# Kernel optimization log

Measured on AMD Instinct MI355X. Metric: run time of the kernel, lower is better.

The kernel has to match this reference:

```python
import jax, jax.numpy as jnp
import numpy as np

D_KQ = 1024

def setup_inputs() -> dict:
    key = jax.random.key(0)
    k1, k2, k3, k4, k5 = jax.random.split(key, 5)
    x = jax.random.normal(k1, (4, 2048, 1024), dtype=jnp.float32)
    attention_mask = jax.random.randint(k2, (2048, 2048), 0, 2) == 1
    q_weights = jax.random.normal(k3, (1024, 1024), dtype=jnp.float32)
    k_weights = jax.random.normal(k4, (1024, 1024), dtype=jnp.float32)
    v_weights = jax.random.normal(k5, (1024, 1024), dtype=jnp.float32)
    return {"x": x, "attention_mask": attention_mask,
            "q_weights": q_weights, "k_weights": k_weights, "v_weights": v_weights}

def reference(x, attention_mask, q_weights, k_weights, v_weights):
    # projections: [B,S,d_in] @ [d_in,d] -> [B,S,d]
    query = x @ q_weights
    key = x @ k_weights
    value = x @ v_weights
    # scores: [B,S,S]
    attn_scores = jnp.einsum('bqd,bkd->bqk', query, key)
    masked = jnp.where(attention_mask, -jnp.inf, attn_scores)
    attn_weights = jax.nn.softmax(masked / jnp.sqrt(jnp.float32(D_KQ)), axis=-1)
    return attn_weights @ value
```

## Files before the change

### kernel.cpp

```cpp
#include <hip/hip_runtime.h>
#include <math.h>

static constexpr int BATCH = 4;
static constexpr int SEQ   = 2048;
static constexpr int DIM   = 1024;

typedef __attribute__((ext_vector_type(8))) short     bf16x8;
typedef __attribute__((ext_vector_type(4))) float     f32x4;

__device__ __forceinline__ unsigned short f2b(float v) {
    unsigned int u = __float_as_uint(v);
    u = u + 0x7fffu + ((u >> 16) & 1u);
    return (unsigned short)(u >> 16);
}
__device__ __forceinline__ float b2f(unsigned short h) {
    return __uint_as_float(((unsigned int)h) << 16);
}

__global__ __launch_bounds__(256) void convert_x_kernel(
    const float* __restrict__ X, unsigned short* __restrict__ hi,
    unsigned short* __restrict__ lo)
{
    const int i = blockIdx.x * 256 + threadIdx.x;
    const float4 v = ((const float4*)X)[i];
    ushort4 h, l;
    h.x = f2b(v.x); l.x = f2b(v.x - b2f(h.x));
    h.y = f2b(v.y); l.y = f2b(v.y - b2f(h.y));
    h.z = f2b(v.z); l.z = f2b(v.z - b2f(h.z));
    h.w = f2b(v.w); l.w = f2b(v.w - b2f(h.w));
    ((ushort4*)hi)[i] = h;
    ((ushort4*)lo)[i] = l;
}

__global__ __launch_bounds__(256) void convert_wqk_kernel(
    const float* __restrict__ Wq, const float* __restrict__ Wk,
    unsigned short* __restrict__ hi, unsigned short* __restrict__ lo)
{
    const int z = blockIdx.y;
    const float* __restrict__ W = z ? Wk : Wq;
    const int i = blockIdx.x * 256 + threadIdx.x;
    const int o = z * (DIM * DIM / 4) + i;
    const float4 v = ((const float4*)W)[i];
    ushort4 h, l;
    h.x = f2b(v.x); l.x = f2b(v.x - b2f(h.x));
    h.y = f2b(v.y); l.y = f2b(v.y - b2f(h.y));
    h.z = f2b(v.z); l.z = f2b(v.z - b2f(h.z));
    h.w = f2b(v.w); l.w = f2b(v.w - b2f(h.w));
    ((ushort4*)hi)[o] = h;
    ((ushort4*)lo)[o] = l;
}

__global__ __launch_bounds__(256) void convert_wv_kernel(
    const float* __restrict__ W, unsigned short* __restrict__ WT)
{
    __shared__ float t[32][33];
    const int n0 = blockIdx.x * 32, k0 = blockIdx.y * 32;
    const int tx = threadIdx.x & 31, ty = threadIdx.x >> 5;
#pragma unroll
    for (int i = 0; i < 4; ++i)
        t[ty + i * 8][tx] = W[(size_t)(k0 + ty + i * 8) * DIM + (n0 + tx)];
    __syncthreads();
#pragma unroll
    for (int i = 0; i < 4; ++i)
        WT[(size_t)(n0 + ty + i * 8) * DIM + (k0 + tx)] = f2b(t[tx][ty + i * 8]);
}

__global__ __launch_bounds__(256) void mask_pack_kernel(
    const int* __restrict__ mask, unsigned long long* __restrict__ Mb)
{
    const int row  = blockIdx.x;
    const int lane = threadIdx.x & 63, w = threadIdx.x >> 6;
#pragma unroll
    for (int c = w; c < SEQ / 64; c += 4) {
        const int v = mask[(size_t)row * SEQ + c * 64 + lane];
        const unsigned long long bits = __ballot(v != 0);
        if (lane == 0) Mb[(size_t)row * (SEQ / 64) + c] = bits;
    }
}

__device__ __forceinline__ void stage_async(
    const unsigned short* __restrict__ g, int gstride, int row0, int k0,
    unsigned short* lds, int tid)
{
    const int w = tid >> 6, lane = tid & 63;
    const int c = (lane & 3) ^ ((lane >> 4) & 3);
#pragma unroll
    for (int h = 0; h < 2; ++h) {
        const int row = 32 * w + 16 * h + (lane >> 2);
        const unsigned short* src = g + (size_t)(row0 + row) * gstride + k0 + 8 * c;
        unsigned short* dst = lds + (32 * w + 16 * h) * 32;
        __builtin_amdgcn_global_load_lds(
            (const __attribute__((address_space(1))) void*)src,
            (__attribute__((address_space(3))) void*)dst, 16, 0, 0);
    }
}

__device__ __forceinline__ void stage128(
    const unsigned short* __restrict__ g, int gstride, int row0, int k0,
    unsigned short* lds, int tid)
{
    const int w = tid >> 6, lane = tid & 63;
    const int c = (lane & 3) ^ ((lane >> 4) & 3);
    const int row = 16 * w + (lane >> 2);
    const unsigned short* src = g + (size_t)(row0 + row) * gstride + k0 + 8 * c;
    unsigned short* dst = lds + (16 * w) * 32;
    __builtin_amdgcn_global_load_lds(
        (const __attribute__((address_space(1))) void*)src,
        (__attribute__((address_space(3))) void*)dst, 16, 0, 0);
}

__device__ __forceinline__ bf16x8 fragr(const unsigned short* lds, int row, int qsw)
{
    return *(const bf16x8*)(lds + row * 32 + qsw * 8);
}

__global__ __launch_bounds__(256) void m_gemm_kernel(
    const unsigned short* __restrict__ Whi, const unsigned short* __restrict__ Wlo,
    float* __restrict__ Mtp)
{
    __shared__ unsigned short Ah[128 * 32], Al[128 * 32];
    __shared__ unsigned short Bh[128 * 32], Bl[128 * 32];

    const int tid = threadIdx.x;
    const int w = tid >> 6, lane = tid & 63;
    const int wm = (w >> 1) * 64, wn = (w & 1) * 64;
    const int m0 = blockIdx.y * 128, n0 = blockIdx.x * 128;
    const int z = blockIdx.z;

    const unsigned short* __restrict__ Ahg = Whi + (size_t)DIM * DIM;
    const unsigned short* __restrict__ Alg = Wlo + (size_t)DIM * DIM;
    const unsigned short* __restrict__ Bhg = Whi;
    const unsigned short* __restrict__ Blg = Wlo;
    float* __restrict__ Cp = Mtp + (size_t)z * DIM * DIM;

    f32x4 acc[4][4];
#pragma unroll
    for (int i = 0; i < 4; ++i)
#pragma unroll
        for (int j = 0; j < 4; ++j) acc[i][j] = (f32x4){0.f, 0.f, 0.f, 0.f};

    const int fr = lane & 15, quad = lane >> 4;
    const int qsw = quad ^ ((fr >> 2) & 3);

    for (int k0 = z * 256; k0 < z * 256 + 256; k0 += 32) {
        stage_async(Ahg, DIM, m0, k0, Ah, tid);
        stage_async(Alg, DIM, m0, k0, Al, tid);
        stage_async(Bhg, DIM, n0, k0, Bh, tid);
        stage_async(Blg, DIM, n0, k0, Bl, tid);
        __syncthreads();

        bf16x8 ah[4], al[4];
#pragma unroll
        for (int mt = 0; mt < 4; ++mt) {
            ah[mt] = fragr(Ah, wm + mt * 16 + fr, qsw);
            al[mt] = fragr(Al, wm + mt * 16 + fr, qsw);
        }
#pragma unroll
        for (int nt = 0; nt < 4; ++nt) {
            const bf16x8 bh = fragr(Bh, wn + nt * 16 + fr, qsw);
            const bf16x8 bl = fragr(Bl, wn + nt * 16 + fr, qsw);
#pragma unroll
            for (int mt = 0; mt < 4; ++mt) {
                acc[mt][nt] = __builtin_amdgcn_mfma_f32_16x16x32_bf16(ah[mt], bh, acc[mt][nt], 0, 0, 0);
                acc[mt][nt] = __builtin_amdgcn_mfma_f32_16x16x32_bf16(ah[mt], bl, acc[mt][nt], 0, 0, 0);
                acc[mt][nt] = __builtin_amdgcn_mfma_f32_16x16x32_bf16(al[mt], bh, acc[mt][nt], 0, 0, 0);
            }
        }
        __syncthreads();
    }

    const int col = lane & 15, rq = lane >> 4;
#pragma unroll
    for (int mt = 0; mt < 4; ++mt)
#pragma unroll
        for (int nt = 0; nt < 4; ++nt)
#pragma unroll
            for (int e = 0; e < 4; ++e) {
                const int m = m0 + wm + mt * 16 + rq * 4 + e;
                const int n = n0 + wn + nt * 16 + col;
                Cp[(size_t)m * DIM + n] = acc[mt][nt][e];
            }
}

__global__ __launch_bounds__(256) void m_reduce_kernel(
    const float* __restrict__ Mtp, unsigned short* __restrict__ Mthi,
    unsigned short* __restrict__ Mtlo)
{
    const int i = blockIdx.x * 256 + threadIdx.x;
    const size_t q = (size_t)DIM * DIM / 4;
    const float4 a = ((const float4*)Mtp)[i];
    const float4 b = ((const float4*)Mtp)[i + q];
    const float4 c = ((const float4*)Mtp)[i + 2 * q];
    const float4 d = ((const float4*)Mtp)[i + 3 * q];
    const float4 v = make_float4(a.x + b.x + c.x + d.x, a.y + b.y + c.y + d.y,
                                 a.z + b.z + c.z + d.z, a.w + b.w + c.w + d.w);
    ushort4 h, l;
    h.x = f2b(v.x); l.x = f2b(v.x - b2f(h.x));
    h.y = f2b(v.y); l.y = f2b(v.y - b2f(h.y));
    h.z = f2b(v.z); l.z = f2b(v.z - b2f(h.z));
    h.w = f2b(v.w); l.w = f2b(v.w - b2f(h.w));
    ((ushort4*)Mthi)[i] = h;
    ((ushort4*)Mtlo)[i] = l;
}

__global__ __launch_bounds__(512, 2) void yv_gemm_kernel(
    const unsigned short* __restrict__ Xhi, const unsigned short* __restrict__ Xlo,
    const unsigned short* __restrict__ Mthi, const unsigned short* __restrict__ Mtlo,
    const unsigned short* __restrict__ WvT,
    unsigned short* __restrict__ Yhi, unsigned short* __restrict__ Ylo,
    unsigned short* __restrict__ Vt)
{
    extern __shared__ unsigned short smem[];

    const int tid = threadIdx.x;
    const int w = tid >> 6, lane = tid & 63;
    const int wm = (w >> 1) * 64, wn = (w & 1) * 64;

    const int flat = blockIdx.x + (blockIdx.y << 3);
    const int xcd = flat & 7, s = flat >> 3;
    const int m0 = (xcd + ((s >> 3) << 3)) * 256;
    const int n0 = (s & 7) * 128;

    f32x4 accY[4][4], accV[4][4];
#pragma unroll
    for (int i = 0; i < 4; ++i)
#pragma unroll
        for (int j = 0; j < 4; ++j) {
            accY[i][j] = (f32x4){0.f, 0.f, 0.f, 0.f};
            accV[i][j] = (f32x4){0.f, 0.f, 0.f, 0.f};
        }

    const int fr = lane & 15, quad = lane >> 4;
    const int qsw = quad ^ ((fr >> 2) & 3);

    stage_async(Xhi, DIM, m0, 0, smem + 0,     tid);
    stage128(Mthi, DIM, n0, 0, smem + 16384, tid);
    stage128(Mtlo, DIM, n0, 0, smem + 20480, tid);
    stage_async(Xlo, DIM, m0, 0, smem + 8192,  tid);
    stage128(WvT,  DIM, n0, 0, smem + 24576, tid);

    bf16x8 ah[4], al[4], bh[4], bl[4], bv[4];

    for (int it = 0; it < DIM / 32 - 1; ++it) {
        const int cur = (it & 1) * 28672;
        const int nxt = 28672 - cur;
        const int k1 = it * 32 + 32;

        stage_async(Xhi, DIM, m0, k1, smem + nxt, tid);
        asm volatile("s_waitcnt vmcnt(6)" ::: "memory");
        __builtin_amdgcn_s_barrier();
#pragma unroll
        for (int mt = 0; mt < 4; ++mt)
            ah[mt] = fragr(smem + cur, wm + mt * 16 + fr, qsw);
#pragma unroll
        for (int nt = 0; nt < 4; ++nt)
            bh[nt] = fragr(smem + cur + 16384, wn + nt * 16 + fr, qsw);
        __builtin_amdgcn_s_setprio(1);
#pragma unroll
        for (int nt = 0; nt < 4; ++nt)
#pragma unroll
            for (int mt = 0; mt < 4; ++mt)
                accY[mt][nt] = __builtin_amdgcn_mfma_f32_16x16x32_bf16(ah[mt], bh[nt], accY[mt][nt], 0, 0, 0);
        __builtin_amdgcn_s_setprio(0);

        stage128(Mthi, DIM, n0, k1, smem + nxt + 16384, tid);
        stage128(Mtlo, DIM, n0, k1, smem + nxt + 20480, tid);
        asm volatile("s_waitcnt vmcnt(7)" ::: "memory");
        __builtin_amdgcn_s_barrier();
#pragma unroll
        for (int nt = 0; nt < 4; ++nt)
            bl[nt] = fragr(smem + cur + 20480, wn + nt * 16 + fr, qsw);
        __builtin_amdgcn_s_setprio(1);
#pragma unroll
        for (int nt = 0; nt < 4; ++nt)
#pragma unroll
            for (int mt = 0; mt < 4; ++mt)
                accY[mt][nt] = __builtin_amdgcn_mfma_f32_16x16x32_bf16(ah[mt], bl[nt], accY[mt][nt], 0, 0, 0);
        __builtin_amdgcn_s_setprio(0);

        stage_async(Xlo, DIM, m0, k1, smem + nxt + 8192, tid);
        asm volatile("s_waitcnt vmcnt(6)" ::: "memory");
        __builtin_amdgcn_s_barrier();
#pragma unroll
        for (int nt = 0; nt < 4; ++nt)
            bv[nt] = fragr(smem + cur + 24576, wn + nt * 16 + fr, qsw);
        __builtin_amdgcn_s_setprio(1);
#pragma unroll
        for (int nt = 0; nt < 4; ++nt)
#pragma unroll
            for (int mt = 0; mt < 4; ++mt)
                accV[mt][nt] = __builtin_amdgcn_mfma_f32_16x16x32_bf16(ah[mt], bv[nt], accV[mt][nt], 0, 0, 0);
        __builtin_amdgcn_s_setprio(0);

        stage128(WvT, DIM, n0, k1, smem + nxt + 24576, tid);
        asm volatile("s_waitcnt vmcnt(8)" ::: "memory");
        __builtin_amdgcn_s_barrier();
#pragma unroll
        for (int mt = 0; mt < 4; ++mt)
            al[mt] = fragr(smem + cur + 8192, wm + mt * 16 + fr, qsw);
        __builtin_amdgcn_s_setprio(1);
#pragma unroll
        for (int nt = 0; nt < 4; ++nt)
#pragma unroll
            for (int mt = 0; mt < 4; ++mt)
                accY[mt][nt] = __builtin_amdgcn_mfma_f32_16x16x32_bf16(al[mt], bh[nt], accY[mt][nt], 0, 0, 0);
        __builtin_amdgcn_s_setprio(0);
    }

    {
        const int cur = 28672;

        asm volatile("s_waitcnt vmcnt(4)" ::: "memory");
        __builtin_amdgcn_s_barrier();
#pragma unroll
        for (int mt = 0; mt < 4; ++mt)
            ah[mt] = fragr(smem + cur, wm + mt * 16 + fr, qsw);
#pragma unroll
        for (int nt = 0; nt < 4; ++nt)
            bh[nt] = fragr(smem + cur + 16384, wn + nt * 16 + fr, qsw);
        __builtin_amdgcn_s_setprio(1);
#pragma unroll
        for (int nt = 0; nt < 4; ++nt)
#pragma unroll
            for (int mt = 0; mt < 4; ++mt)
                accY[mt][nt] = __builtin_amdgcn_mfma_f32_16x16x32_bf16(ah[mt], bh[nt], accY[mt][nt], 0, 0, 0);
        __builtin_amdgcn_s_setprio(0);

        asm volatile("s_waitcnt vmcnt(3)" ::: "memory");
        __builtin_amdgcn_s_barrier();
#pragma unroll
        for (int nt = 0; nt < 4; ++nt)
            bl[nt] = fragr(smem + cur + 20480, wn + nt * 16 + fr, qsw);
        __builtin_amdgcn_s_setprio(1);
#pragma unroll
        for (int nt = 0; nt < 4; ++nt)
#pragma unroll
            for (int mt = 0; mt < 4; ++mt)
                accY[mt][nt] = __builtin_amdgcn_mfma_f32_16x16x32_bf16(ah[mt], bl[nt], accY[mt][nt], 0, 0, 0);
        __builtin_amdgcn_s_setprio(0);

        asm volatile("s_waitcnt vmcnt(0)" ::: "memory");
        __builtin_amdgcn_s_barrier();
#pragma unroll
        for (int nt = 0; nt < 4; ++nt)
            bv[nt] = fragr(smem + cur + 24576, wn + nt * 16 + fr, qsw);
        __builtin_amdgcn_s_setprio(1);
#pragma unroll
        for (int nt = 0; nt < 4; ++nt)
#pragma unroll
            for (int mt = 0; mt < 4; ++mt)
                accV[mt][nt] = __builtin_amdgcn_mfma_f32_16x16x32_bf16(ah[mt], bv[nt], accV[mt][nt], 0, 0, 0);
        __builtin_amdgcn_s_setprio(0);

#pragma unroll
        for (int mt = 0; mt < 4; ++mt)
            al[mt] = fragr(smem + cur + 8192, wm + mt * 16 + fr, qsw);
        __builtin_amdgcn_s_setprio(1);
#pragma unroll
        for (int nt = 0; nt < 4; ++nt)
#pragma unroll
            for (int mt = 0; mt < 4; ++mt)
                accY[mt][nt] = __builtin_amdgcn_mfma_f32_16x16x32_bf16(al[mt], bh[nt], accY[mt][nt], 0, 0, 0);
        __builtin_amdgcn_s_setprio(0);
    }

    const int col = lane & 15, rq = lane >> 4;
#pragma unroll
    for (int mt = 0; mt < 4; ++mt)
#pragma unroll
        for (int nt = 0; nt < 4; ++nt)
#pragma unroll
            for (int e = 0; e < 4; ++e) {
                const int m = m0 + wm + mt * 16 + rq * 4 + e;
                const int n = n0 + wn + nt * 16 + col;
                const float v = accY[mt][nt][e];
                const unsigned short h = f2b(v);
                Yhi[(size_t)m * DIM + n] = h;
                Ylo[(size_t)m * DIM + n] = f2b(v - b2f(h));
            }
#pragma unroll
    for (int mt = 0; mt < 4; ++mt)
#pragma unroll
        for (int nt = 0; nt < 4; ++nt) {
            const int m = m0 + wm + mt * 16 + rq * 4;
            const int bb = m >> 11, sr = m & (SEQ - 1);
            const int n = n0 + wn + nt * 16 + col;
            ushort4 pk;
            pk.x = f2b(accV[mt][nt][0]);
            pk.y = f2b(accV[mt][nt][1]);
            pk.z = f2b(accV[mt][nt][2]);
            pk.w = f2b(accV[mt][nt][3]);
            *(ushort4*)(Vt + (size_t)bb * DIM * SEQ + (size_t)n * SEQ + sr) = pk;
        }
}

__global__ __launch_bounds__(512, 2) void s_gemm256_kernel(
    const unsigned short* __restrict__ Yhi, const unsigned short* __restrict__ Ylo,
    const unsigned short* __restrict__ Xhi, const unsigned short* __restrict__ Xlo,
    const unsigned long long* __restrict__ Mb, float* __restrict__ Sc)
{
    extern __shared__ unsigned short smem[];

    const int tid = threadIdx.x;
    const int w = tid >> 6, lane = tid & 63;
    const int wm = (w >> 2) * 128, wn = (w & 3) * 64;

    const int flat = blockIdx.x + (blockIdx.y << 3) + (blockIdx.z << 6);
    const int lid  = ((flat & 7) << 5) | (flat >> 3);
    const int m0 = ((lid >> 3) & 7) * 256, n0 = (lid & 7) * 256;
    const int b  = lid >> 6;

    const unsigned short* __restrict__ Ahg = Yhi + (size_t)b * SEQ * DIM;
    const unsigned short* __restrict__ Alg = Ylo + (size_t)b * SEQ * DIM;
    const unsigned short* __restrict__ Bhg = Xhi + (size_t)b * SEQ * DIM;
    const unsigned short* __restrict__ Blg = Xlo + (size_t)b * SEQ * DIM;
    float* __restrict__ Sb = Sc + (size_t)b * SEQ * SEQ;

    f32x4 acc[8][4];
#pragma unroll
    for (int i = 0; i < 8; ++i)
#pragma unroll
        for (int j = 0; j < 4; ++j) acc[i][j] = (f32x4){0.f, 0.f, 0.f, 0.f};

    const int fr = lane & 15, quad = lane >> 4;
    const int qsw = quad ^ ((fr >> 2) & 3);

    stage_async(Ahg, DIM, m0, 0, smem + 0,     tid);
    stage_async(Bhg, DIM, n0, 0, smem + 16384, tid);
    stage_async(Blg, DIM, n0, 0, smem + 24576, tid);
    stage_async(Alg, DIM, m0, 0, smem + 8192,  tid);

    for (int it = 0; it < DIM / 32 - 1; ++it) {
        const int cur = (it & 1) * 32768;
        const int nxt = cur ^ 32768;
        const unsigned short* Ah = smem + cur;
        const unsigned short* Al = smem + cur + 8192;
        const unsigned short* Bh = smem + cur + 16384;
        const unsigned short* Bl = smem + cur + 24576;
        const int k1 = it * 32 + 32;

        bf16x8 ah[8], al[8], bh[4], bl[4];

        stage_async(Ahg, DIM, m0, k1, smem + nxt, tid);
        asm volatile("s_waitcnt vmcnt(6)" ::: "memory");
        __builtin_amdgcn_s_barrier();
#pragma unroll
        for (int mt = 0; mt < 4; ++mt)
            ah[mt] = fragr(Ah, wm + mt * 16 + fr, qsw);
#pragma unroll
        for (int nt = 0; nt < 4; ++nt)
            bh[nt] = fragr(Bh, wn + nt * 16 + fr, qsw);
        __builtin_amdgcn_s_setprio(1);
#pragma unroll
        for (int nt = 0; nt < 4; ++nt)
#pragma unroll
            for (int mt = 0; mt < 4; ++mt)
                acc[mt][nt] = __builtin_amdgcn_mfma_f32_16x16x32_bf16(ah[mt], bh[nt], acc[mt][nt], 0, 0, 0);
        __builtin_amdgcn_s_setprio(0);

        stage_async(Bhg, DIM, n0, k1, smem + nxt + 16384, tid);
#pragma unroll
        for (int mt = 4; mt < 8; ++mt)
            ah[mt] = fragr(Ah, wm + mt * 16 + fr, qsw);
        __builtin_amdgcn_s_setprio(1);
#pragma unroll
        for (int nt = 0; nt < 4; ++nt)
#pragma unroll
            for (int mt = 4; mt < 8; ++mt)
                acc[mt][nt] = __builtin_amdgcn_mfma_f32_16x16x32_bf16(ah[mt], bh[nt], acc[mt][nt], 0, 0, 0);
        __builtin_amdgcn_s_setprio(0);

        stage_async(Blg, DIM, n0, k1, smem + nxt + 24576, tid);
        asm volatile("s_waitcnt vmcnt(8)" ::: "memory");
        __builtin_amdgcn_s_barrier();
#pragma unroll
        for (int nt = 0; nt < 4; ++nt)
            bl[nt] = fragr(Bl, wn + nt * 16 + fr, qsw);
        __builtin_amdgcn_s_setprio(1);
#pragma unroll
        for (int nt = 0; nt < 4; ++nt)
#pragma unroll
            for (int mt = 0; mt < 4; ++mt)
                acc[mt][nt] = __builtin_amdgcn_mfma_f32_16x16x32_bf16(ah[mt], bl[nt], acc[mt][nt], 0, 0, 0);
        __builtin_amdgcn_s_setprio(0);

        __builtin_amdgcn_s_setprio(1);
#pragma unroll
        for (int nt = 0; nt < 4; ++nt)
#pragma unroll
            for (int mt = 4; mt < 8; ++mt)
                acc[mt][nt] = __builtin_amdgcn_mfma_f32_16x16x32_bf16(ah[mt], bl[nt], acc[mt][nt], 0, 0, 0);
        __builtin_amdgcn_s_setprio(0);

        stage_async(Alg, DIM, m0, k1, smem + nxt + 8192, tid);
        asm volatile("s_waitcnt vmcnt(8)" ::: "memory");
        __builtin_amdgcn_s_barrier();
#pragma unroll
        for (int mt = 0; mt < 4; ++mt)
            al[mt] = fragr(Al, wm + mt * 16 + fr, qsw);
        __builtin_amdgcn_s_setprio(1);
#pragma unroll
        for (int nt = 0; nt < 4; ++nt)
#pragma unroll
            for (int mt = 0; mt < 4; ++mt)
                acc[mt][nt] = __builtin_amdgcn_mfma_f32_16x16x32_bf16(al[mt], bh[nt], acc[mt][nt], 0, 0, 0);
        __builtin_amdgcn_s_setprio(0);

#pragma unroll
        for (int mt = 4; mt < 8; ++mt)
            al[mt] = fragr(Al, wm + mt * 16 + fr, qsw);
        __builtin_amdgcn_s_setprio(1);
#pragma unroll
        for (int nt = 0; nt < 4; ++nt)
#pragma unroll
            for (int mt = 4; mt < 8; ++mt)
                acc[mt][nt] = __builtin_amdgcn_mfma_f32_16x16x32_bf16(al[mt], bh[nt], acc[mt][nt], 0, 0, 0);
        __builtin_amdgcn_s_setprio(0);
    }

    {
        const unsigned short* Ah = smem + 32768;
        const unsigned short* Al = smem + 32768 + 8192;
        const unsigned short* Bh = smem + 32768 + 16384;
        const unsigned short* Bl = smem + 32768 + 24576;

        bf16x8 ah[8], al[8], bh[4], bl[4];

        asm volatile("s_waitcnt vmcnt(4)" ::: "memory");
        __builtin_amdgcn_s_barrier();
#pragma unroll
        for (int mt = 0; mt < 8; ++mt)
            ah[mt] = fragr(Ah, wm + mt * 16 + fr, qsw);
#pragma unroll
        for (int nt = 0; nt < 4; ++nt)
            bh[nt] = fragr(Bh, wn + nt * 16 + fr, qsw);
        __builtin_amdgcn_s_setprio(1);
#pragma unroll
        for (int nt = 0; nt < 4; ++nt)
#pragma unroll
            for (int mt = 0; mt < 8; ++mt)
                acc[mt][nt] = __builtin_amdgcn_mfma_f32_16x16x32_bf16(ah[mt], bh[nt], acc[mt][nt], 0, 0, 0);
        __builtin_amdgcn_s_setprio(0);

        asm volatile("s_waitcnt vmcnt(2)" ::: "memory");
        __builtin_amdgcn_s_barrier();
#pragma unroll
        for (int nt = 0; nt < 4; ++nt)
            bl[nt] = fragr(Bl, wn + nt * 16 + fr, qsw);
        __builtin_amdgcn_s_setprio(1);
#pragma unroll
        for (int nt = 0; nt < 4; ++nt)
#pragma unroll
            for (int mt = 0; mt < 8; ++mt)
                acc[mt][nt] = __builtin_amdgcn_mfma_f32_16x16x32_bf16(ah[mt], bl[nt], acc[mt][nt], 0, 0, 0);
        __builtin_amdgcn_s_setprio(0);

        asm volatile("s_waitcnt vmcnt(0)" ::: "memory");
        __builtin_amdgcn_s_barrier();
#pragma unroll
        for (int mt = 0; mt < 8; ++mt)
            al[mt] = fragr(Al, wm + mt * 16 + fr, qsw);
        __builtin_amdgcn_s_setprio(1);
#pragma unroll
        for (int nt = 0; nt < 4; ++nt)
#pragma unroll
            for (int mt = 0; mt < 8; ++mt)
                acc[mt][nt] = __builtin_amdgcn_mfma_f32_16x16x32_bf16(al[mt], bh[nt], acc[mt][nt], 0, 0, 0);
        __builtin_amdgcn_s_setprio(0);
    }

    const int col = lane & 15, rq = lane >> 4;
    const int wword = (n0 + wn) >> 6;
#pragma unroll
    for (int mt = 0; mt < 8; ++mt)
#pragma unroll
        for (int e = 0; e < 4; ++e) {
            const int m = m0 + wm + mt * 16 + rq * 4 + e;
            const unsigned long long word = Mb[(size_t)m * (SEQ / 64) + wword];
#pragma unroll
            for (int nt = 0; nt < 4; ++nt) {
                const int n = n0 + wn + nt * 16 + col;
                const float v = acc[mt][nt][e] * 0.03125f;
                const bool msk = (word >> (nt * 16 + col)) & 1ull;
                Sb[(size_t)m * SEQ + n] = msk ? -INFINITY : v;
            }
        }
}

__global__ __launch_bounds__(256) void softmax_kernel(float* __restrict__ Sc)
{
    const int r = blockIdx.x;
    float* __restrict__ row = Sc + (size_t)r * SEQ;

    const int tid  = threadIdx.x;
    const int lane = tid & 63;
    const int wid  = tid >> 6;

    float x[8];
    float mx = -INFINITY;
#pragma unroll
    for (int j = 0; j < 8; ++j) {
        x[j] = row[tid + j * 256];
        mx = fmaxf(mx, x[j]);
    }
    __shared__ float redm[4];
#pragma unroll
    for (int off = 32; off > 0; off >>= 1)
        mx = fmaxf(mx, __shfl_down(mx, off, 64));
    if (lane == 0) redm[wid] = mx;
    __syncthreads();
    mx = fmaxf(fmaxf(redm[0], redm[1]), fmaxf(redm[2], redm[3]));

    float sum = 0.f;
#pragma unroll
    for (int j = 0; j < 8; ++j) {
        const float e = __expf(x[j] - mx);
        x[j] = e;
        sum += e;
    }
    __shared__ float reds[4];
#pragma unroll
    for (int off = 32; off > 0; off >>= 1)
        sum += __shfl_down(sum, off, 64);
    if (lane == 0) reds[wid] = sum;
    __syncthreads();
    sum = (reds[0] + reds[1]) + (reds[2] + reds[3]);

    const float inv = 1.0f / sum;
    unsigned short* __restrict__ prow = (unsigned short*)row;
#pragma unroll
    for (int j = 0; j < 8; ++j)
        prow[tid + j * 256] = f2b(x[j] * inv);
}

__global__ __launch_bounds__(256) void pv_mfma_kernel(
    const unsigned short* __restrict__ P, const unsigned short* __restrict__ Vt,
    float* __restrict__ O)
{
    __shared__ unsigned short As[2][128 * 32], Bs[2][128 * 32];

    const int tid = threadIdx.x;
    const int w = tid >> 6, lane = tid & 63;
    const int wm = (w >> 1) * 64, wn = (w & 1) * 64;

    const int flat = blockIdx.x + (blockIdx.y << 3) + (blockIdx.z << 7);
    const int lid  = ((flat & 7) << 6) | (flat >> 3);
    const int m0 = ((lid >> 3) & 15) * 128, n0 = (lid & 7) * 128;
    const int b  = lid >> 7;

    const unsigned short* __restrict__ Ag = P + (size_t)b * SEQ * (2 * SEQ);
    const unsigned short* __restrict__ Bg = Vt + (size_t)b * DIM * SEQ;
    float* __restrict__ Ob = O + (size_t)b * SEQ * DIM;

    f32x4 acc[4][4];
#pragma unroll
    for (int i = 0; i < 4; ++i)
#pragma unroll
        for (int j = 0; j < 4; ++j) acc[i][j] = (f32x4){0.f, 0.f, 0.f, 0.f};

    const int fr = lane & 15, quad = lane >> 4;
    const int qsw = quad ^ ((fr >> 2) & 3);

    stage_async(Ag, 2 * SEQ, m0, 0, As[0], tid);
    stage_async(Bg, SEQ,     n0, 0, Bs[0], tid);

    for (int it = 0; it < SEQ / 32 - 1; ++it) {
        const int cur = it & 1, nxt = cur ^ 1;
        const int k1 = it * 32 + 32;

        stage_async(Ag, 2 * SEQ, m0, k1, As[nxt], tid);
        stage_async(Bg, SEQ,     n0, k1, Bs[nxt], tid);
        asm volatile("s_waitcnt vmcnt(4)" ::: "memory");
        __builtin_amdgcn_s_barrier();

        bf16x8 af[4];
#pragma unroll
        for (int mt = 0; mt < 4; ++mt)
            af[mt] = fragr(As[cur], wm + mt * 16 + fr, qsw);
        __builtin_amdgcn_s_setprio(1);
#pragma unroll
        for (int nt = 0; nt < 4; ++nt) {
            const bf16x8 bfg = fragr(Bs[cur], wn + nt * 16 + fr, qsw);
#pragma unroll
            for (int mt = 0; mt < 4; ++mt)
                acc[mt][nt] = __builtin_amdgcn_mfma_f32_16x16x32_bf16(af[mt], bfg, acc[mt][nt], 0, 0, 0);
        }
        __builtin_amdgcn_s_setprio(0);
        __builtin_amdgcn_s_barrier();
    }

    {
        asm volatile("s_waitcnt vmcnt(0)" ::: "memory");
        __builtin_amdgcn_s_barrier();
        bf16x8 af[4];
#pragma unroll
        for (int mt = 0; mt < 4; ++mt)
            af[mt] = fragr(As[1], wm + mt * 16 + fr, qsw);
        __builtin_amdgcn_s_setprio(1);
#pragma unroll
        for (int nt = 0; nt < 4; ++nt) {
            const bf16x8 bfg = fragr(Bs[1], wn + nt * 16 + fr, qsw);
#pragma unroll
            for (int mt = 0; mt < 4; ++mt)
                acc[mt][nt] = __builtin_amdgcn_mfma_f32_16x16x32_bf16(af[mt], bfg, acc[mt][nt], 0, 0, 0);
        }
        __builtin_amdgcn_s_setprio(0);
    }

    const int col = lane & 15, rq = lane >> 4;
#pragma unroll
    for (int mt = 0; mt < 4; ++mt)
#pragma unroll
        for (int nt = 0; nt < 4; ++nt)
#pragma unroll
            for (int e = 0; e < 4; ++e) {
                const int m = m0 + wm + mt * 16 + rq * 4 + e;
                const int n = n0 + wn + nt * 16 + col;
                Ob[(size_t)m * DIM + n] = acc[mt][nt][e];
            }
}

extern "C" void kernel_launch(void* const* d_in, const int* in_sizes, int n_in,
                              void* d_out, int out_size, void* d_ws, size_t ws_size,
                              hipStream_t stream)
{
    const float* x    = (const float*)d_in[0];
    const int*   mask = (const int*)d_in[1];
    const float* wq   = (const float*)d_in[2];
    const float* wk   = (const float*)d_in[3];
    const float* wv   = (const float*)d_in[4];
    float* out = (float*)d_out;

    const size_t NQ = (size_t)BATCH * SEQ * DIM;
    const size_t NM = (size_t)DIM * DIM;
    unsigned short* Xhi  = (unsigned short*)d_ws;
    unsigned short* Xlo  = Xhi + NQ;
    unsigned short* Yhi  = Xlo + NQ;
    unsigned short* Ylo  = Yhi + NQ;
    unsigned short* Vt   = Ylo + NQ;
    unsigned short* Mthi = Vt + NQ;
    unsigned short* Mtlo = Mthi + NM;
    float* Sc = (float*)(Mtlo + NM);
    unsigned long long* Mb = (unsigned long long*)(Sc + (size_t)BATCH * SEQ * SEQ);

    unsigned short* Whi = (unsigned short*)Sc;
    unsigned short* Wlo = Whi + 2 * NM;
    unsigned short* WvT = Wlo + 2 * NM;
    float* Mtp = (float*)(WvT + NM);

    static bool lds_attr_set = false;
    if (!lds_attr_set) {
        (void)hipFuncSetAttribute((const void*)s_gemm256_kernel,
                                  hipFuncAttributeMaxDynamicSharedMemorySize,
                                  131072);
        (void)hipFuncSetAttribute((const void*)yv_gemm_kernel,
                                  hipFuncAttributeMaxDynamicSharedMemorySize,
                                  114688);
        lds_attr_set = true;
    }

    convert_x_kernel<<<dim3(NQ / 4 / 256), 256, 0, stream>>>(x, Xhi, Xlo);
    mask_pack_kernel<<<dim3(SEQ), 256, 0, stream>>>(mask, Mb);
    convert_wqk_kernel<<<dim3(NM / 4 / 256, 2), 256, 0, stream>>>(wq, wk, Whi, Wlo);
    convert_wv_kernel<<<dim3(32, 32), 256, 0, stream>>>(wv, WvT);
    m_gemm_kernel<<<dim3(8, 8, 4), 256, 0, stream>>>(Whi, Wlo, Mtp);
    m_reduce_kernel<<<dim3(NM / 4 / 256), 256, 0, stream>>>(Mtp, Mthi, Mtlo);
    yv_gemm_kernel<<<dim3(DIM / 128, (BATCH * SEQ) / 256), 512, 114688, stream>>>(
        Xhi, Xlo, Mthi, Mtlo, WvT, Yhi, Ylo, Vt);
    s_gemm256_kernel<<<dim3(SEQ / 256, SEQ / 256, BATCH), 512, 131072, stream>>>(
        Yhi, Ylo, Xhi, Xlo, Mb, Sc);
    softmax_kernel<<<dim3(BATCH * SEQ), 256, 0, stream>>>(Sc);
    pv_mfma_kernel<<<dim3(DIM / 128, SEQ / 128, BATCH), 256, 0, stream>>>(
        (const unsigned short*)Sc, Vt, out);
}
```

Measured before the change: 354.3 us.

## Enlarge PV tiles with triple-buffered staging and vectorize softmax row access

```diff
diff --git a/kernel.cpp b/kernel.cpp
--- a/kernel.cpp
+++ b/kernel.cpp
@@ -596,13 +596,13 @@
     const int lane = tid & 63;
     const int wid  = tid >> 6;
 
-    float x[8];
+    const float4 v0 = ((const float4*)row)[2 * tid];
+    const float4 v1 = ((const float4*)row)[2 * tid + 1];
+    float x[8] = {v0.x, v0.y, v0.z, v0.w, v1.x, v1.y, v1.z, v1.w};
+
     float mx = -INFINITY;
 #pragma unroll
-    for (int j = 0; j < 8; ++j) {
-        x[j] = row[tid + j * 256];
-        mx = fmaxf(mx, x[j]);
-    }
+    for (int j = 0; j < 8; ++j) mx = fmaxf(mx, x[j]);
     __shared__ float redm[4];
 #pragma unroll
     for (int off = 32; off > 0; off >>= 1)
@@ -628,25 +628,29 @@
 
     const float inv = 1.0f / sum;
     unsigned short* __restrict__ prow = (unsigned short*)row;
+    bf16x8 pk;
 #pragma unroll
     for (int j = 0; j < 8; ++j)
-        prow[tid + j * 256] = f2b(x[j] * inv);
-}
-
-__global__ __launch_bounds__(256) void pv_mfma_kernel(
+        pk[j] = (short)f2b(x[j] * inv);
+    *(bf16x8*)(prow + 8 * tid) = pk;
+}
+
+__global__ __launch_bounds__(512, 2) void pv_mfma_kernel(
     const unsigned short* __restrict__ P, const unsigned short* __restrict__ Vt,
     float* __restrict__ O)
 {
-    __shared__ unsigned short As[2][128 * 32], Bs[2][128 * 32];
+    __shared__ unsigned short As[3][256 * 32], Bs[3][128 * 32];
 
     const int tid = threadIdx.x;
     const int w = tid >> 6, lane = tid & 63;
     const int wm = (w >> 1) * 64, wn = (w & 1) * 64;
 
-    const int flat = blockIdx.x + (blockIdx.y << 3) + (blockIdx.z << 7);
-    const int lid  = ((flat & 7) << 6) | (flat >> 3);
-    const int m0 = ((lid >> 3) & 15) * 128, n0 = (lid & 7) * 128;
-    const int b  = lid >> 7;
+    const int flat = blockIdx.x + (blockIdx.y << 3) + (blockIdx.z << 6);
+    const int xcd = flat & 7, s = flat >> 3;
+    const int c  = xcd + ((s >> 3) << 3);
+    const int n0 = (s & 7) * 128;
+    const int m0 = (c & 7) * 256;
+    const int b  = c >> 3;
 
     const unsigned short* __restrict__ Ag = P + (size_t)b * SEQ * (2 * SEQ);
     const unsigned short* __restrict__ Bg = Vt + (size_t)b * DIM * SEQ;
@@ -662,48 +666,49 @@
     const int qsw = quad ^ ((fr >> 2) & 3);
 
     stage_async(Ag, 2 * SEQ, m0, 0, As[0], tid);
-    stage_async(Bg, SEQ,     n0, 0, Bs[0], tid);
+    stage128 (Bg, SEQ,      n0, 0, Bs[0], tid);
 
     for (int it = 0; it < SEQ / 32 - 1; ++it) {
-        const int cur = it & 1, nxt = cur ^ 1;
+        const int cur = it % 3, nxt = (it + 1) % 3;
         const int k1 = it * 32 + 32;
 
         stage_async(Ag, 2 * SEQ, m0, k1, As[nxt], tid);
-        stage_async(Bg, SEQ,     n0, k1, Bs[nxt], tid);
-        asm volatile("s_waitcnt vmcnt(4)" ::: "memory");
-        __builtin_amdgcn_s_barrier();
-
-        bf16x8 af[4];
+        stage128 (Bg, SEQ,      n0, k1, Bs[nxt], tid);
+        asm volatile("s_waitcnt vmcnt(3)" ::: "memory");
+        __builtin_amdgcn_s_barrier();
+
+        bf16x8 af[4], bfv[4];
 #pragma unroll
         for (int mt = 0; mt < 4; ++mt)
             af[mt] = fragr(As[cur], wm + mt * 16 + fr, qsw);
-        __builtin_amdgcn_s_setprio(1);
-#pragma unroll
-        for (int nt = 0; nt < 4; ++nt) {
-            const bf16x8 bfg = fragr(Bs[cur], wn + nt * 16 + fr, qsw);
-#pragma unroll
-            for (int mt = 0; mt < 4; ++mt)
-                acc[mt][nt] = __builtin_amdgcn_mfma_f32_16x16x32_bf16(af[mt], bfg, acc[mt][nt], 0, 0, 0);
-        }
-        __builtin_amdgcn_s_setprio(0);
-        __builtin_amdgcn_s_barrier();
+#pragma unroll
+        for (int nt = 0; nt < 4; ++nt)
+            bfv[nt] = fragr(Bs[cur], wn + nt * 16 + fr, qsw);
+        __builtin_amdgcn_s_setprio(1);
+#pragma unroll
+        for (int nt = 0; nt < 4; ++nt)
+#pragma unroll
+            for (int mt = 0; mt < 4; ++mt)
+                acc[mt][nt] = __builtin_amdgcn_mfma_f32_16x16x32_bf16(af[mt], bfv[nt], acc[mt][nt], 0, 0, 0);
+        __builtin_amdgcn_s_setprio(0);
     }
 
     {
         asm volatile("s_waitcnt vmcnt(0)" ::: "memory");
         __builtin_amdgcn_s_barrier();
-        bf16x8 af[4];
+        bf16x8 af[4], bfv[4];
 #pragma unroll
         for (int mt = 0; mt < 4; ++mt)
-            af[mt] = fragr(As[1], wm + mt * 16 + fr, qsw);
-        __builtin_amdgcn_s_setprio(1);
-#pragma unroll
-        for (int nt = 0; nt < 4; ++nt) {
-            const bf16x8 bfg = fragr(Bs[1], wn + nt * 16 + fr, qsw);
-#pragma unroll
-            for (int mt = 0; mt < 4; ++mt)
-                acc[mt][nt] = __builtin_amdgcn_mfma_f32_16x16x32_bf16(af[mt], bfg, acc[mt][nt], 0, 0, 0);
-        }
+            af[mt] = fragr(As[0], wm + mt * 16 + fr, qsw);
+#pragma unroll
+        for (int nt = 0; nt < 4; ++nt)
+            bfv[nt] = fragr(Bs[0], wn + nt * 16 + fr, qsw);
+        __builtin_amdgcn_s_setprio(1);
+#pragma unroll
+        for (int nt = 0; nt < 4; ++nt)
+#pragma unroll
+            for (int mt = 0; mt < 4; ++mt)
+                acc[mt][nt] = __builtin_amdgcn_mfma_f32_16x16x32_bf16(af[mt], bfv[nt], acc[mt][nt], 0, 0, 0);
         __builtin_amdgcn_s_setprio(0);
     }
 
@@ -770,6 +775,6 @@
     s_gemm256_kernel<<<dim3(SEQ / 256, SEQ / 256, BATCH), 512, 131072, stream>>>(
         Yhi, Ylo, Xhi, Xlo, Mb, Sc);
     softmax_kernel<<<dim3(BATCH * SEQ), 256, 0, stream>>>(Sc);
-    pv_mfma_kernel<<<dim3(DIM / 128, SEQ / 128, BATCH), 256, 0, stream>>>(
+    pv_mfma_kernel<<<dim3(DIM / 128, SEQ / 256, BATCH), 512, 0, stream>>>(
         (const unsigned short*)Sc, Vt, out);
 }
```

Result: no change. 352.0 us (-0.7%).
